# Kernel optimization log

Measured on AMD Instinct MI355X. Metric: run time of the kernel, lower is better.

## Reference

```python
import jax, jax.numpy as jnp
import numpy as np

N, FEAT, NCLS = 8192, 1024, 64


def setup_inputs() -> dict:
    key = jax.random.key(0)
    k1, k2, k3, k4, k5, k6 = jax.random.split(key, 6)
    x = jax.random.normal(k1, (N, FEAT), dtype=jnp.float32)
    adj = jax.random.uniform(k2, (N, N), dtype=jnp.float32)  # pairwise distances
    stdv1 = 1.0 / np.sqrt(FEAT)
    W1 = jax.random.uniform(k3, (FEAT, FEAT), jnp.float32, -stdv1, stdv1)
    b1 = jax.random.uniform(k4, (FEAT,), jnp.float32, -stdv1, stdv1)
    W2 = jax.random.uniform(k5, (FEAT, NCLS), jnp.float32, -stdv1, stdv1)
    b2 = jax.random.uniform(k6, (NCLS,), jnp.float32, -stdv1, stdv1)
    alpha = jnp.full((1,), 0.3, dtype=jnp.float32)
    return {"x": x, "adj": adj, "W1": W1, "b1": b1, "W2": W2, "b2": b2,
            "alpha": alpha, "K": 32}


def reference(x, adj, W1, b1, W2, b2, alpha, K):
    # --- top-K smallest-distance neighbor selection per row ---
    neg_vals, idx = jax.lax.top_k(-adj, K)        # K smallest adj entries per row
    vals = -neg_vals                              # [N, K] distances
    w = jnp.exp(-alpha[0] * vals)                 # 1 / exp(alpha * d)
    w = w / jnp.sum(w, axis=1, keepdims=True)     # row-normalize edge weights

    def spmm(h):
        # sparse A @ h using top-K edge list: out[i] = sum_k w[i,k] * h[idx[i,k]]
        return jnp.einsum('nk,nkf->nf', w, h[idx])

    # 2-layer GCN path of SimTSC (eval mode: dropout is identity)
    h = jax.nn.relu(spmm(x @ W1) + b1)            # [N, FEAT]
    out = spmm(h @ W2) + b2                       # [N, NCLS]
    return jax.nn.log_softmax(out, axis=1)
```

## Files before the change

### kernel.cpp

```cpp
#include <hip/hip_runtime.h>

typedef __bf16 bf16_t;
typedef __bf16 bf16x4 __attribute__((ext_vector_type(4)));
typedef __bf16 bf16x8 __attribute__((ext_vector_type(8)));
typedef float  f32x4  __attribute__((ext_vector_type(4)));

typedef const __attribute__((address_space(1))) void gvoid_t;
typedef __attribute__((address_space(3))) void lvoid_t;

#define N_NODES 8192
#define FEAT    1024
#define NCLS    64
#define TK      32

__device__ __forceinline__ float wave_min_f32(float v) {
  int x = __float_as_int(v), t;
#define STEPF(ctrl) t = __builtin_amdgcn_update_dpp(x, x, ctrl, 0xf, 0xf, false); \
                    v = fminf(v, __int_as_float(t)); x = __float_as_int(v);
  STEPF(0x111)
  STEPF(0x112)
  STEPF(0x114)
  STEPF(0x118)
  STEPF(0x142)
  STEPF(0x143)
#undef STEPF
  return __int_as_float(__builtin_amdgcn_readlane(x, 63));
}

__device__ __forceinline__ unsigned wave_min_u32(unsigned v) {
  int x = (int)v, t;
#define STEPU(ctrl) t = __builtin_amdgcn_update_dpp(x, x, ctrl, 0xf, 0xf, false); \
                    x = (int)((unsigned)x < (unsigned)t ? (unsigned)x : (unsigned)t);
  STEPU(0x111)
  STEPU(0x112)
  STEPU(0x114)
  STEPU(0x118)
  STEPU(0x142)
  STEPU(0x143)
#undef STEPU
  return (unsigned)__builtin_amdgcn_readlane(x, 63);
}

__global__ __launch_bounds__(256) void topk_kernel(const float* __restrict__ adj,
                                                   const float* __restrict__ alphap,
                                                   int* __restrict__ idx_out,
                                                   float* __restrict__ w_out,
                                                   const float* __restrict__ W1,
                                                   bf16_t* __restrict__ W1t,
                                                   const float* __restrict__ W2,
                                                   bf16_t* __restrict__ W2t) {
  const int tid = threadIdx.x;
  __shared__ float tile[64][65];
  __shared__ float svals[256];
  __shared__ int   sidx[256];
  __shared__ int   scnt;

  if (blockIdx.x >= N_NODES) {
    const int tb = blockIdx.x - N_NODES;
    const int bxi = tb % 17, by = tb / 17;
    const float* in;
    bf16_t* out;
    int cols, bx;
    if (bxi < 16) { in = W1; out = W1t; cols = FEAT; bx = bxi; }
    else          { in = W2; out = W2t; cols = NCLS; bx = 0; }
#pragma unroll
    for (int i = 0; i < 16; ++i) {
      int li = i * 256 + tid;
      int r = li >> 6, c = li & 63;
      tile[r][c] = in[(size_t)(by * 64 + r) * cols + bx * 64 + c];
    }
    __syncthreads();
#pragma unroll
    for (int i = 0; i < 16; ++i) {
      int li = i * 256 + tid;
      int r = li >> 6, c = li & 63;
      out[(size_t)(bx * 64 + r) * FEAT + by * 64 + c] = (__bf16)tile[c][r];
    }
    return;
  }

  const int row = blockIdx.x;
  const float* arow = adj + (size_t)row * N_NODES;
  float thr = 1.0f / 128.0f;
  int cnt = 0;
  for (int attempt = 0; attempt < 24; ++attempt) {
    __syncthreads();
    if (tid == 0) scnt = 0;
    __syncthreads();
#pragma unroll
    for (int v = 0; v < 8; ++v) {
      int vi = v * 256 + tid;
      float4 q = ((const float4*)arow)[vi];
      int base = vi * 4;
      if (q.x < thr) { int p = atomicAdd(&scnt, 1); if (p < 256) { svals[p] = q.x; sidx[p] = base;     } }
      if (q.y < thr) { int p = atomicAdd(&scnt, 1); if (p < 256) { svals[p] = q.y; sidx[p] = base + 1; } }
      if (q.z < thr) { int p = atomicAdd(&scnt, 1); if (p < 256) { svals[p] = q.z; sidx[p] = base + 2; } }
      if (q.w < thr) { int p = atomicAdd(&scnt, 1); if (p < 256) { svals[p] = q.w; sidx[p] = base + 3; } }
    }
    __syncthreads();
    cnt = scnt;
    if (cnt >= TK && cnt <= 256) break;
    thr = (cnt < TK) ? thr * 2.0f : thr * 0.5f;
  }
  const int M = cnt < 256 ? cnt : 256;

  if (tid < 64) {
    const int lane = tid;
    const float INF = __int_as_float(0x7f800000);
    float cv[4];
    int   ci[4];
#pragma unroll
    for (int j = 0; j < 4; ++j) {
      int slot = lane + j * 64;
      if (slot < M) { cv[j] = svals[slot]; ci[j] = sidx[slot]; }
      else          { cv[j] = INF;         ci[j] = 0x7fffffff; }
    }
    float selv = 0.f;
    int   seli = 0;
    for (int k = 0; k < TK; ++k) {
      const float lv = fminf(fminf(cv[0], cv[1]), fminf(cv[2], cv[3]));
      const float wv = wave_min_f32(lv);
      unsigned li = 0xffffffffu;
#pragma unroll
      for (int j = 0; j < 4; ++j)
        if (cv[j] == wv) li = li < (unsigned)ci[j] ? li : (unsigned)ci[j];
      const unsigned wi = wave_min_u32(li);
      if (lane == k) { selv = wv; seli = (int)wi; }
#pragma unroll
      for (int j = 0; j < 4; ++j)
        if (cv[j] == wv && (unsigned)ci[j] == wi) cv[j] = INF;
    }
    const float a = alphap[0];
    const float e = (lane < TK) ? expf(-a * selv) : 0.0f;
    float ssum = e;
#pragma unroll
    for (int off = 1; off < 64; off <<= 1) ssum += __shfl_xor(ssum, off);
    if (lane < TK) {
      idx_out[(size_t)row * TK + lane] = seli & (N_NODES - 1);
      w_out[(size_t)row * TK + lane]   = e / ssum;
    }
  }
}

__global__ __launch_bounds__(256, 2) void gemm1_kernel(const float* __restrict__ A,
                                                       const bf16_t* __restrict__ Bt,
                                                       bf16_t* __restrict__ C) {
  constexpr int BM = 128, BN = 128, Kd = FEAT;
  constexpr int LDSA = BM * 64;
  constexpr int LDSB = BN * 64;
  __shared__ char lds[2][LDSA + LDSB];
  const int tid = threadIdx.x;
  const int wid = tid >> 6, lane = tid & 63;
  const int b = blockIdx.x;
  const int xcd = b & 7, j = b >> 3;
  const int bm0 = (xcd * 8 + (j >> 3)) * BM;
  const int bn0 = (j & 7) * BN;
  const int wr = wid >> 1, wc = wid & 1;
  constexpr int WM = BM / 2, WN = BN / 2;
  constexpr int NMI = WM / 16, NNI = WN / 16;

  auto stageA = [&](int buf, int t) {
    const int k0 = t * 32;
#pragma unroll
    for (int it = 0; it < 2; ++it) {
      const int i = it * 256 + tid;
      const int r = i >> 2, g = i & 3;
      const float* src = A + (size_t)(bm0 + r) * Kd + k0 + g * 8;
      const float4 f0 = ((const float4*)src)[0];
      const float4 f1 = ((const float4*)src)[1];
      bf16x8 o;
      o[0] = (__bf16)f0.x; o[1] = (__bf16)f0.y; o[2] = (__bf16)f0.z; o[3] = (__bf16)f0.w;
      o[4] = (__bf16)f1.x; o[5] = (__bf16)f1.y; o[6] = (__bf16)f1.z; o[7] = (__bf16)f1.w;
      *(bf16x8*)(&lds[buf][r * 64 + ((g ^ (r & 3)) * 16)]) = o;
    }
  };
  auto stageB = [&](int buf, int t) {
    const int k0 = t * 32;
#pragma unroll
    for (int li = 0; li < BN / 64; ++li) {
      const int rb = wid * (BN / 4) + li * 16;
      const int r = rb + (lane >> 2);
      const int sdat = (lane & 3) ^ (r & 3);
      const bf16_t* g = Bt + (size_t)(bn0 + r) * Kd + k0 + sdat * 8;
      __builtin_amdgcn_global_load_lds((gvoid_t*)g, (lvoid_t*)&lds[buf][LDSA + rb * 64], 16, 0, 0);
    }
  };

  f32x4 acc[NMI][NNI];
#pragma unroll
  for (int mi = 0; mi < NMI; ++mi)
#pragma unroll
    for (int ni = 0; ni < NNI; ++ni) acc[mi][ni] = (f32x4){0.f, 0.f, 0.f, 0.f};

  const int nT = Kd / 32;
  stageB(0, 0);
  stageA(0, 0);
  __syncthreads();
  for (int t = 0; t < nT; ++t) {
    const int cur = t & 1;
    if (t + 1 < nT) { stageB(cur ^ 1, t + 1); stageA(cur ^ 1, t + 1); }
    const char* la = &lds[cur][0];
    const char* lb = &lds[cur][LDSA];
    const int s = lane >> 4;
    bf16x8 af[NMI], bfr[NNI];
#pragma unroll
    for (int mi = 0; mi < NMI; ++mi) {
      const int m = wr * WM + mi * 16 + (lane & 15);
      af[mi] = *(const bf16x8*)(la + m * 64 + ((s ^ (m & 3)) * 16));
    }
#pragma unroll
    for (int ni = 0; ni < NNI; ++ni) {
      const int n = wc * WN + ni * 16 + (lane & 15);
      bfr[ni] = *(const bf16x8*)(lb + n * 64 + ((s ^ (n & 3)) * 16));
    }
#pragma unroll
    for (int mi = 0; mi < NMI; ++mi)
#pragma unroll
      for (int ni = 0; ni < NNI; ++ni)
        acc[mi][ni] = __builtin_amdgcn_mfma_f32_16x16x32_bf16(af[mi], bfr[ni], acc[mi][ni], 0, 0, 0);
    __syncthreads();
  }

#pragma unroll
  for (int mi = 0; mi < NMI; ++mi)
#pragma unroll
    for (int ni = 0; ni < NNI; ++ni)
#pragma unroll
      for (int j4 = 0; j4 < 4; ++j4) {
        const int r = bm0 + wr * WM + mi * 16 + (lane >> 4) * 4 + j4;
        const int c = bn0 + wc * WN + ni * 16 + (lane & 15);
        C[(size_t)r * FEAT + c] = (__bf16)acc[mi][ni][j4];
      }
}

#define SROWS  16
#define SCHUNK 128
#define NCHUNK 8
__global__ __launch_bounds__(256) void spmm_gemm2_kernel(const bf16_t* __restrict__ xW1,
                                                         const int* __restrict__ idxm,
                                                         const float* __restrict__ wm,
                                                         const float* __restrict__ b1,
                                                         const bf16_t* __restrict__ W2t,
                                                         float* __restrict__ part) {
  const int tid = threadIdx.x;
  const int c  = blockIdx.x & (NCHUNK - 1);
  const int rg = blockIdx.x >> 3;
  const int r0 = rg * SROWS;
  const int f0 = c * SCHUNK;
  __shared__ int    snb[SROWS][TK];
  __shared__ float  swt[SROWS][TK];
  __shared__ bf16_t hls[SROWS][SCHUNK];
  ((int2*)&snb[0][0])[tid]   = ((const int2*)(idxm + (size_t)r0 * TK))[tid];
  ((float2*)&swt[0][0])[tid] = ((const float2*)(wm + (size_t)r0 * TK))[tid];
  __syncthreads();
  const int wid = tid >> 6, lane = tid & 63;
  const int gr = tid >> 4;
  const int gc = (tid & 15) * 8;

  float a[8];
#pragma unroll
  for (int j = 0; j < 8; ++j) a[j] = 0.f;
#pragma unroll 8
  for (int k = 0; k < TK; ++k) {
    const bf16x8 v = *(const bf16x8*)(xW1 + (size_t)snb[gr][k] * FEAT + f0 + gc);
    const float wk = swt[gr][k];
#pragma unroll
    for (int j = 0; j < 8; ++j) a[j] += wk * (float)v[j];
  }
  const float4 b0 = ((const float4*)(b1 + f0 + gc))[0];
  const float4 b1v = ((const float4*)(b1 + f0 + gc))[1];
  bf16x8 o0;
  o0[0] = (__bf16)fmaxf(a[0] + b0.x, 0.f);
  o0[1] = (__bf16)fmaxf(a[1] + b0.y, 0.f);
  o0[2] = (__bf16)fmaxf(a[2] + b0.z, 0.f);
  o0[3] = (__bf16)fmaxf(a[3] + b0.w, 0.f);
  o0[4] = (__bf16)fmaxf(a[4] + b1v.x, 0.f);
  o0[5] = (__bf16)fmaxf(a[5] + b1v.y, 0.f);
  o0[6] = (__bf16)fmaxf(a[6] + b1v.z, 0.f);
  o0[7] = (__bf16)fmaxf(a[7] + b1v.w, 0.f);
  const int g0 = (gc >> 3);
  char* hb = (char*)&hls[0][0];
  *(bf16x8*)(hb + gr * (SCHUNK * 2) + ((g0 ^ (gr & 7)) * 16)) = o0;

  const int s = lane >> 4;
  const int m = lane & 15;
  const int n = wid * 16 + (lane & 15);
  bf16x8 bfr[SCHUNK / 32];
#pragma unroll
  for (int ks = 0; ks < SCHUNK / 32; ++ks)
    bfr[ks] = *(const bf16x8*)(W2t + (size_t)n * FEAT + f0 + ks * 32 + s * 8);
  __syncthreads();

  f32x4 acc = (f32x4){0.f, 0.f, 0.f, 0.f};
  const char* hr = (char*)&hls[0][0] + m * (SCHUNK * 2);
#pragma unroll
  for (int ks = 0; ks < SCHUNK / 32; ++ks) {
    const int g = ks * 4 + s;
    const bf16x8 afrag = *(const bf16x8*)(hr + ((g ^ (m & 7)) * 16));
    acc = __builtin_amdgcn_mfma_f32_16x16x32_bf16(afrag, bfr[ks], acc, 0, 0, 0);
  }
#pragma unroll
  for (int j = 0; j < 4; ++j) {
    const int r = r0 + (lane >> 4) * 4 + j;
    const int col = wid * 16 + (lane & 15);
    part[((size_t)c * N_NODES + r) * NCLS + col] = acc[j];
  }
}

__global__ __launch_bounds__(256) void reduce8_kernel(const float* __restrict__ part,
                                                      float* __restrict__ out2) {
  const int i = blockIdx.x * 256 + threadIdx.x;
  float4 s = ((const float4*)(part))[i];
#pragma unroll
  for (int c = 1; c < NCHUNK; ++c) {
    const float4 p = ((const float4*)(part + (size_t)c * N_NODES * NCLS))[i];
    s.x += p.x; s.y += p.y; s.z += p.z; s.w += p.w;
  }
  ((float4*)out2)[i] = s;
}

__global__ __launch_bounds__(256) void final_kernel(const float* __restrict__ out2,
                                                    const int* __restrict__ idxm,
                                                    const float* __restrict__ wm,
                                                    const float* __restrict__ b2,
                                                    float* __restrict__ out) {
  const int wid = threadIdx.x >> 6, lane = threadIdx.x & 63;
  const int row = blockIdx.x * 4 + wid;
  const int kk = lane & 31;
  const float wv = wm[(size_t)row * TK + kk];
  const int   iv = idxm[(size_t)row * TK + kk];
  float acc = 0.f;
#pragma unroll 8
  for (int k = 0; k < TK; ++k) {
    const float wk = __shfl(wv, k);
    const int   ik = __shfl(iv, k);
    acc += wk * out2[(size_t)ik * NCLS + lane];
  }
  const float logit = acc + b2[lane];
  float m = logit;
#pragma unroll
  for (int off = 1; off < 64; off <<= 1) m = fmaxf(m, __shfl_xor(m, off));
  const float e = expf(logit - m);
  float ssum = e;
#pragma unroll
  for (int off = 1; off < 64; off <<= 1) ssum += __shfl_xor(ssum, off);
  out[(size_t)row * NCLS + lane] = (logit - m) - logf(ssum);
}

extern "C" void kernel_launch(void* const* d_in, const int* in_sizes, int n_in,
                              void* d_out, int out_size, void* d_ws, size_t ws_size,
                              hipStream_t stream) {
  (void)in_sizes; (void)n_in; (void)out_size; (void)ws_size;
  const float* x     = (const float*)d_in[0];
  const float* adj   = (const float*)d_in[1];
  const float* W1    = (const float*)d_in[2];
  const float* b1    = (const float*)d_in[3];
  const float* W2    = (const float*)d_in[4];
  const float* b2    = (const float*)d_in[5];
  const float* alpha = (const float*)d_in[6];

  char* ws = (char*)d_ws;
  const size_t MB = 1024 * 1024;
  bf16_t* xW1  = (bf16_t*)(ws + 16 * MB);
  bf16_t* W1t  = (bf16_t*)(ws + 48 * MB);
  bf16_t* W2t  = (bf16_t*)(ws + 50 * MB);
  float*  out2 = (float*)(ws + 51 * MB);
  int*    idxm = (int*)(ws + 53 * MB);
  float*  wm   = (float*)(ws + 54 * MB);
  float*  part = (float*)(ws + 56 * MB);

  topk_kernel<<<dim3(N_NODES + 272), dim3(256), 0, stream>>>(
      adj, alpha, idxm, wm, W1, W1t, W2, W2t);
  gemm1_kernel<<<dim3(512), dim3(256), 0, stream>>>(x, W1t, xW1);
  spmm_gemm2_kernel<<<dim3((N_NODES / SROWS) * NCHUNK), dim3(256), 0, stream>>>(
      xW1, idxm, wm, b1, W2t, part);
  reduce8_kernel<<<dim3(N_NODES * NCLS / 4 / 256), dim3(256), 0, stream>>>(part, out2);
  final_kernel<<<dim3(N_NODES / 4), dim3(256), 0, stream>>>(out2, idxm, wm, b2, (float*)d_out);
}
```

Baseline: 149.0 us.

## Fuse top-K selection and first GEMM into one launch to overlap them

The weight transpose/convert moves into its own small kernel. The x@W1 GEMM and the per-row top-K selection now share one fused launch: the first 512 blocks do the GEMM and the rest do top-K. The aim is to overlap the compute-bound GEMM with the bandwidth-bound adj scan and to save one launch. In exchange, the top-K blocks now carry the GEMM's large LDS footprint and launch bounds, which may reduce their occupancy. The XCD-aware block remapping for the GEMM is also dropped.

```diff
diff --git a/kernel.cpp b/kernel.cpp
--- a/kernel.cpp
+++ b/kernel.cpp
@@ -41,64 +41,154 @@
   return (unsigned)__builtin_amdgcn_readlane(x, 63);
 }
 
-__global__ __launch_bounds__(256) void topk_kernel(const float* __restrict__ adj,
-                                                   const float* __restrict__ alphap,
-                                                   int* __restrict__ idx_out,
-                                                   float* __restrict__ w_out,
-                                                   const float* __restrict__ W1,
-                                                   bf16_t* __restrict__ W1t,
-                                                   const float* __restrict__ W2,
-                                                   bf16_t* __restrict__ W2t) {
+__global__ __launch_bounds__(256) void transpose_cvt_kernel(const float* __restrict__ W1,
+                                                            bf16_t* __restrict__ W1t,
+                                                            const float* __restrict__ W2,
+                                                            bf16_t* __restrict__ W2t) {
+  __shared__ float tile[64][65];
+  const float* in;
+  bf16_t* out;
+  int cols, bx;
+  if (blockIdx.x < 16) { in = W1; out = W1t; cols = FEAT; bx = blockIdx.x; }
+  else                 { in = W2; out = W2t; cols = NCLS; bx = 0; }
+  const int by = blockIdx.y;
   const int tid = threadIdx.x;
-  __shared__ float tile[64][65];
-  __shared__ float svals[256];
-  __shared__ int   sidx[256];
-  __shared__ int   scnt;
-
-  if (blockIdx.x >= N_NODES) {
-    const int tb = blockIdx.x - N_NODES;
-    const int bxi = tb % 17, by = tb / 17;
-    const float* in;
-    bf16_t* out;
-    int cols, bx;
-    if (bxi < 16) { in = W1; out = W1t; cols = FEAT; bx = bxi; }
-    else          { in = W2; out = W2t; cols = NCLS; bx = 0; }
-#pragma unroll
-    for (int i = 0; i < 16; ++i) {
-      int li = i * 256 + tid;
-      int r = li >> 6, c = li & 63;
-      tile[r][c] = in[(size_t)(by * 64 + r) * cols + bx * 64 + c];
-    }
+#pragma unroll
+  for (int i = 0; i < 16; ++i) {
+    int li = i * 256 + tid;
+    int r = li >> 6, c = li & 63;
+    tile[r][c] = in[(size_t)(by * 64 + r) * cols + bx * 64 + c];
+  }
+  __syncthreads();
+#pragma unroll
+  for (int i = 0; i < 16; ++i) {
+    int li = i * 256 + tid;
+    int r = li >> 6, c = li & 63;
+    out[(size_t)(bx * 64 + r) * FEAT + by * 64 + c] = (__bf16)tile[c][r];
+  }
+}
+
+#define GEMM_BLOCKS 512
+__global__ __launch_bounds__(256, 2) void fused_kernel(const float* __restrict__ adj,
+                                                       const float* __restrict__ alphap,
+                                                       const float* __restrict__ x,
+                                                       const bf16_t* __restrict__ W1t,
+                                                       bf16_t* __restrict__ xW1,
+                                                       int* __restrict__ idx_out,
+                                                       float* __restrict__ w_out) {
+  constexpr int BM = 128, BN = 128;
+  constexpr int LDSA = BM * 64;
+  constexpr int LDSB = BN * 64;
+  __shared__ char lds[2][LDSA + LDSB];
+  const int tid = threadIdx.x;
+
+  if (blockIdx.x < GEMM_BLOCKS) {
+    const int j = blockIdx.x;
+    const int bm0 = (j >> 3) * BM;
+    const int bn0 = (j & 7) * BN;
+    const int wid = tid >> 6, lane = tid & 63;
+    const int wr = wid >> 1, wc = wid & 1;
+    constexpr int WM = BM / 2, WN = BN / 2;
+    constexpr int NMI = WM / 16, NNI = WN / 16;
+
+    auto stageA = [&](int buf, int t) {
+      const int k0 = t * 32;
+#pragma unroll
+      for (int it = 0; it < 2; ++it) {
+        const int i = it * 256 + tid;
+        const int r = i >> 2, g = i & 3;
+        const float* src = x + (size_t)(bm0 + r) * FEAT + k0 + g * 8;
+        const float4 f0 = ((const float4*)src)[0];
+        const float4 f1 = ((const float4*)src)[1];
+        bf16x8 o;
+        o[0] = (__bf16)f0.x; o[1] = (__bf16)f0.y; o[2] = (__bf16)f0.z; o[3] = (__bf16)f0.w;
+        o[4] = (__bf16)f1.x; o[5] = (__bf16)f1.y; o[6] = (__bf16)f1.z; o[7] = (__bf16)f1.w;
+        *(bf16x8*)(&lds[buf][r * 64 + ((g ^ (r & 3)) * 16)]) = o;
+      }
+    };
+    auto stageB = [&](int buf, int t) {
+      const int k0 = t * 32;
+#pragma unroll
+      for (int li = 0; li < BN / 64; ++li) {
+        const int rb = wid * (BN / 4) + li * 16;
+        const int r = rb + (lane >> 2);
+        const int sdat = (lane & 3) ^ (r & 3);
+        const bf16_t* g = W1t + (size_t)(bn0 + r) * FEAT + k0 + sdat * 8;
+        __builtin_amdgcn_global_load_lds((gvoid_t*)g, (lvoid_t*)&lds[buf][LDSA + rb * 64], 16, 0, 0);
+      }
+    };
+
+    f32x4 acc[NMI][NNI];
+#pragma unroll
+    for (int mi = 0; mi < NMI; ++mi)
+#pragma unroll
+      for (int ni = 0; ni < NNI; ++ni) acc[mi][ni] = (f32x4){0.f, 0.f, 0.f, 0.f};
+
+    const int nT = FEAT / 32;
+    stageB(0, 0);
+    stageA(0, 0);
     __syncthreads();
-#pragma unroll
-    for (int i = 0; i < 16; ++i) {
-      int li = i * 256 + tid;
-      int r = li >> 6, c = li & 63;
-      out[(size_t)(bx * 64 + r) * FEAT + by * 64 + c] = (__bf16)tile[c][r];
-    }
+    for (int t = 0; t < nT; ++t) {
+      const int cur = t & 1;
+      if (t + 1 < nT) { stageB(cur ^ 1, t + 1); stageA(cur ^ 1, t + 1); }
+      const char* la = &lds[cur][0];
+      const char* lb = &lds[cur][LDSA];
+      const int s = lane >> 4;
+      bf16x8 af[NMI], bfr[NNI];
+#pragma unroll
+      for (int mi = 0; mi < NMI; ++mi) {
+        const int m = wr * WM + mi * 16 + (lane & 15);
+        af[mi] = *(const bf16x8*)(la + m * 64 + ((s ^ (m & 3)) * 16));
+      }
+#pragma unroll
+      for (int ni = 0; ni < NNI; ++ni) {
+        const int n = wc * WN + ni * 16 + (lane & 15);
+        bfr[ni] = *(const bf16x8*)(lb + n * 64 + ((s ^ (n & 3)) * 16));
+      }
+#pragma unroll
+      for (int mi = 0; mi < NMI; ++mi)
+#pragma unroll
+        for (int ni = 0; ni < NNI; ++ni)
+          acc[mi][ni] = __builtin_amdgcn_mfma_f32_16x16x32_bf16(af[mi], bfr[ni], acc[mi][ni], 0, 0, 0);
+      __syncthreads();
+    }
+
+#pragma unroll
+    for (int mi = 0; mi < NMI; ++mi)
+#pragma unroll
+      for (int ni = 0; ni < NNI; ++ni)
+#pragma unroll
+        for (int j4 = 0; j4 < 4; ++j4) {
+          const int r = bm0 + wr * WM + mi * 16 + (lane >> 4) * 4 + j4;
+          const int c = bn0 + wc * WN + ni * 16 + (lane & 15);
+          xW1[(size_t)r * FEAT + c] = (__bf16)acc[mi][ni][j4];
+        }
     return;
   }
 
-  const int row = blockIdx.x;
+  float* svals = (float*)&lds[0][0];
+  int*   sidx  = (int*)&lds[0][1024];
+  int*   scnt  = (int*)&lds[0][2048];
+  const int row = blockIdx.x - GEMM_BLOCKS;
   const float* arow = adj + (size_t)row * N_NODES;
   float thr = 1.0f / 128.0f;
   int cnt = 0;
   for (int attempt = 0; attempt < 24; ++attempt) {
     __syncthreads();
-    if (tid == 0) scnt = 0;
+    if (tid == 0) *scnt = 0;
     __syncthreads();
 #pragma unroll
     for (int v = 0; v < 8; ++v) {
       int vi = v * 256 + tid;
       float4 q = ((const float4*)arow)[vi];
       int base = vi * 4;
-      if (q.x < thr) { int p = atomicAdd(&scnt, 1); if (p < 256) { svals[p] = q.x; sidx[p] = base;     } }
-      if (q.y < thr) { int p = atomicAdd(&scnt, 1); if (p < 256) { svals[p] = q.y; sidx[p] = base + 1; } }
-      if (q.z < thr) { int p = atomicAdd(&scnt, 1); if (p < 256) { svals[p] = q.z; sidx[p] = base + 2; } }
-      if (q.w < thr) { int p = atomicAdd(&scnt, 1); if (p < 256) { svals[p] = q.w; sidx[p] = base + 3; } }
+      if (q.x < thr) { int p = atomicAdd(scnt, 1); if (p < 256) { svals[p] = q.x; sidx[p] = base;     } }
+      if (q.y < thr) { int p = atomicAdd(scnt, 1); if (p < 256) { svals[p] = q.y; sidx[p] = base + 1; } }
+      if (q.z < thr) { int p = atomicAdd(scnt, 1); if (p < 256) { svals[p] = q.z; sidx[p] = base + 2; } }
+      if (q.w < thr) { int p = atomicAdd(scnt, 1); if (p < 256) { svals[p] = q.w; sidx[p] = base + 3; } }
     }
     __syncthreads();
-    cnt = scnt;
+    cnt = *scnt;
     if (cnt >= TK && cnt <= 256) break;
     thr = (cnt < TK) ? thr * 2.0f : thr * 0.5f;
   }
@@ -140,97 +230,6 @@
       w_out[(size_t)row * TK + lane]   = e / ssum;
     }
   }
-}
-
-__global__ __launch_bounds__(256, 2) void gemm1_kernel(const float* __restrict__ A,
-                                                       const bf16_t* __restrict__ Bt,
-                                                       bf16_t* __restrict__ C) {
-  constexpr int BM = 128, BN = 128, Kd = FEAT;
-  constexpr int LDSA = BM * 64;
-  constexpr int LDSB = BN * 64;
-  __shared__ char lds[2][LDSA + LDSB];
-  const int tid = threadIdx.x;
-  const int wid = tid >> 6, lane = tid & 63;
-  const int b = blockIdx.x;
-  const int xcd = b & 7, j = b >> 3;
-  const int bm0 = (xcd * 8 + (j >> 3)) * BM;
-  const int bn0 = (j & 7) * BN;
-  const int wr = wid >> 1, wc = wid & 1;
-  constexpr int WM = BM / 2, WN = BN / 2;
-  constexpr int NMI = WM / 16, NNI = WN / 16;
-
-  auto stageA = [&](int buf, int t) {
-    const int k0 = t * 32;
-#pragma unroll
-    for (int it = 0; it < 2; ++it) {
-      const int i = it * 256 + tid;
-      const int r = i >> 2, g = i & 3;
-      const float* src = A + (size_t)(bm0 + r) * Kd + k0 + g * 8;
-      const float4 f0 = ((const float4*)src)[0];
-      const float4 f1 = ((const float4*)src)[1];
-      bf16x8 o;
-      o[0] = (__bf16)f0.x; o[1] = (__bf16)f0.y; o[2] = (__bf16)f0.z; o[3] = (__bf16)f0.w;
-      o[4] = (__bf16)f1.x; o[5] = (__bf16)f1.y; o[6] = (__bf16)f1.z; o[7] = (__bf16)f1.w;
-      *(bf16x8*)(&lds[buf][r * 64 + ((g ^ (r & 3)) * 16)]) = o;
-    }
-  };
-  auto stageB = [&](int buf, int t) {
-    const int k0 = t * 32;
-#pragma unroll
-    for (int li = 0; li < BN / 64; ++li) {
-      const int rb = wid * (BN / 4) + li * 16;
-      const int r = rb + (lane >> 2);
-      const int sdat = (lane & 3) ^ (r & 3);
-      const bf16_t* g = Bt + (size_t)(bn0 + r) * Kd + k0 + sdat * 8;
-      __builtin_amdgcn_global_load_lds((gvoid_t*)g, (lvoid_t*)&lds[buf][LDSA + rb * 64], 16, 0, 0);
-    }
-  };
-
-  f32x4 acc[NMI][NNI];
-#pragma unroll
-  for (int mi = 0; mi < NMI; ++mi)
-#pragma unroll
-    for (int ni = 0; ni < NNI; ++ni) acc[mi][ni] = (f32x4){0.f, 0.f, 0.f, 0.f};
-
-  const int nT = Kd / 32;
-  stageB(0, 0);
-  stageA(0, 0);
-  __syncthreads();
-  for (int t = 0; t < nT; ++t) {
-    const int cur = t & 1;
-    if (t + 1 < nT) { stageB(cur ^ 1, t + 1); stageA(cur ^ 1, t + 1); }
-    const char* la = &lds[cur][0];
-    const char* lb = &lds[cur][LDSA];
-    const int s = lane >> 4;
-    bf16x8 af[NMI], bfr[NNI];
-#pragma unroll
-    for (int mi = 0; mi < NMI; ++mi) {
-      const int m = wr * WM + mi * 16 + (lane & 15);
-      af[mi] = *(const bf16x8*)(la + m * 64 + ((s ^ (m & 3)) * 16));
-    }
-#pragma unroll
-    for (int ni = 0; ni < NNI; ++ni) {
-      const int n = wc * WN + ni * 16 + (lane & 15);
-      bfr[ni] = *(const bf16x8*)(lb + n * 64 + ((s ^ (n & 3)) * 16));
-    }
-#pragma unroll
-    for (int mi = 0; mi < NMI; ++mi)
-#pragma unroll
-      for (int ni = 0; ni < NNI; ++ni)
-        acc[mi][ni] = __builtin_amdgcn_mfma_f32_16x16x32_bf16(af[mi], bfr[ni], acc[mi][ni], 0, 0, 0);
-    __syncthreads();
-  }
-
-#pragma unroll
-  for (int mi = 0; mi < NMI; ++mi)
-#pragma unroll
-    for (int ni = 0; ni < NNI; ++ni)
-#pragma unroll
-      for (int j4 = 0; j4 < 4; ++j4) {
-        const int r = bm0 + wr * WM + mi * 16 + (lane >> 4) * 4 + j4;
-        const int c = bn0 + wc * WN + ni * 16 + (lane & 15);
-        C[(size_t)r * FEAT + c] = (__bf16)acc[mi][ni][j4];
-      }
 }
 
 #define SROWS  16
@@ -369,9 +368,9 @@
   float*  wm   = (float*)(ws + 54 * MB);
   float*  part = (float*)(ws + 56 * MB);
 
-  topk_kernel<<<dim3(N_NODES + 272), dim3(256), 0, stream>>>(
-      adj, alpha, idxm, wm, W1, W1t, W2, W2t);
-  gemm1_kernel<<<dim3(512), dim3(256), 0, stream>>>(x, W1t, xW1);
+  transpose_cvt_kernel<<<dim3(17, 16), dim3(256), 0, stream>>>(W1, W1t, W2, W2t);
+  fused_kernel<<<dim3(GEMM_BLOCKS + N_NODES), dim3(256), 0, stream>>>(
+      adj, alpha, x, W1t, xW1, idxm, wm);
   spmm_gemm2_kernel<<<dim3((N_NODES / SROWS) * NCHUNK), dim3(256), 0, stream>>>(
       xW1, idxm, wm, b1, W2t, part);
   reduce8_kernel<<<dim3(N_NODES * NCLS / 4 / 256), dim3(256), 0, stream>>>(part, out2);
```

Result: slower. 173.8 us (+16.6%).
